# Optimization experiments

Hardware: AMD Instinct MI355X
Metric: run time of the kernel (lower is better)

Reference implementation:

```python
import jax, jax.numpy as jnp
import numpy as np

B, V, NB, K = 4, 5023, 10, 9
# (Cin, Cout) per NLayer: encoder Linear(3->16) then 3 encoder NLayers, 3 decoder NLayers, Linear(3->3)
CH = [(16, 16), (16, 16), (16, 32), (32, 16), (16, 16), (16, 3)]


def _glorot(key, shape):
    fan_in, fan_out = shape[0], shape[-1]
    s = np.float32(np.sqrt(2.0 / (fan_in + fan_out)))
    return (jax.random.normal(key, shape, dtype=jnp.float32) * s)


def setup_inputs():
    key = jax.random.key(0)
    ks = jax.random.split(key, 4 + 4 * len(CH))
    inp = {}
    inp["x"] = jax.random.normal(ks[0], (B, V, 3), dtype=jnp.float32)
    inp["adj"] = jax.random.randint(ks[1], (V, NB), 0, V + 1, dtype=jnp.int32)
    inp["Win"] = _glorot(ks[2], (3, CH[0][0]))
    inp["Wout"] = _glorot(ks[3], (CH[-1][1], 3))
    for i, (cin, cout) in enumerate(CH):
        k0, k1, k2, k3 = ks[4 + 4 * i], ks[5 + 4 * i], ks[6 + 4 * i], ks[7 + 4 * i]
        inp[f"W{i}"] = _glorot(k0, (cin, K, cout))
        inp[f"b{i}"] = jax.random.normal(k1, (cout,), dtype=jnp.float32) * 0.01
        inp[f"u{i}"] = _glorot(k2, (cin, K))
        inp[f"c{i}"] = jax.random.normal(k3, (K,), dtype=jnp.float32) * 0.01
    return inp


def _pad_gather(t, adj):
    # t: [B, V, ...]; pad a zero row at vertex index 0, gather neighbor features.
    z = jnp.zeros(t.shape[:1] + (1,) + t.shape[2:], t.dtype)
    return jnp.take(jnp.concatenate([z, t], axis=1), adj, axis=1)  # [B, V, NB, ...]


def _nlayer(h, adj, recip, W, b, u, c):
    # h: [B, V, Cin], W: [Cin, K, Cout], u: [Cin, K]
    wx = jnp.einsum('bvc,cko->bvko', h, W)          # [B, V, K, Cout]
    nb_w = _pad_gather(wx, adj)                      # [B, V, NB, K, Cout]
    ux = jnp.einsum('bvc,ck->bvk', h, u)             # [B, V, K]  (u and v maps share self.u)
    nb_u = _pad_gather(ux, adj)                      # [B, V, NB, K]
    q = jax.nn.softmax(ux[:, :, None, :] + nb_u + c, axis=-1)  # softmax over kernel dim
    out = jnp.einsum('bvnk,bvnko->bvo', q, nb_w)     # sum over neighbors & kernels
    return out * recip[None, :, None] + b


def reference(x, adj, Win, Wout, W0, b0, u0, c0, W1, b1, u1, c1, W2, b2, u2, c2,
              W3, b3, u3, c3, W4, b4, u4, c4, W5, b5, u5, c5):
    cnt = jnp.sum(adj != 0, axis=-1).astype(jnp.float32)        # [V]
    recip = jnp.where(cnt > 0, 1.0 / jnp.maximum(cnt, 1.0), 0.0)
    h = jax.nn.relu(x @ Win)
    layers = [(W0, b0, u0, c0), (W1, b1, u1, c1), (W2, b2, u2, c2),
              (W3, b3, u3, c3), (W4, b4, u4, c4), (W5, b5, u5, c5)]
    for (W, b, u, c) in layers:
        h = jax.nn.relu(_nlayer(h, adj, recip, W, b, u, c))
    return h @ Wout
```

## Files before the change

kernel.cpp:

```cpp
#include <hip/hip_runtime.h>

#define NBK 10
#define KK  9

constexpr int Bv  = 4;
constexpr int Vv  = 5023;
constexpr int TOT = Bv * Vv;


__device__ __forceinline__ float merge16(float* a, int t)
{
#pragma unroll
    for (int j = 0; j < 8; j++) {
        float send = (t & 8) ? a[j] : a[j + 8];
        float keep = (t & 8) ? a[j + 8] : a[j];
        a[j] = keep + __shfl_xor(send, 8, 16);
    }
#pragma unroll
    for (int j = 0; j < 4; j++) {
        float send = (t & 4) ? a[j] : a[j + 4];
        float keep = (t & 4) ? a[j + 4] : a[j];
        a[j] = keep + __shfl_xor(send, 4, 16);
    }
#pragma unroll
    for (int j = 0; j < 2; j++) {
        float send = (t & 2) ? a[j] : a[j + 2];
        float keep = (t & 2) ? a[j + 2] : a[j];
        a[j] = keep + __shfl_xor(send, 2, 16);
    }
    {
        float send = (t & 1) ? a[0] : a[1];
        float keep = (t & 1) ? a[1] : a[0];
        a[0] = keep + __shfl_xor(send, 1, 16);
    }
    return a[0];
}

__global__ __launch_bounds__(256, 4) void enc_l0_kernel(
    const float* __restrict__ x,
    const int*   __restrict__ adj,
    const float* __restrict__ Win,
    const float* __restrict__ u0,
    const float* __restrict__ W,
    const float* __restrict__ bvec,
    const float* __restrict__ cvec,
    const float* __restrict__ unx,
    float* __restrict__ hux_out)
{
    constexpr int COUTP = 20;
    __shared__ __align__(16) float s_w[KK * 16 * COUTP];

    const int tid = threadIdx.x;

    {
        constexpr int NF4 = 16 * KK * 16 / 4;
        constexpr int KC4 = KK * 16 / 4;
        const float4* W4 = reinterpret_cast<const float4*>(W);
        for (int i = tid; i < NF4; i += 256) {
            const int c   = i / KC4;
            const int rem = i - c * KC4;
            const int k   = rem >> 2;
            const int o4  = rem & 3;
            *reinterpret_cast<float4*>(&s_w[(k * 16 + c) * COUTP + o4 * 4]) = W4[i];
        }
    }
    __syncthreads();

    const int g = tid >> 4;
    const int t = tid & 15;
    const int vv = blockIdx.x * 16 + g;
    if (vv >= TOT) return;
    const int b = vv / Vv;
    const int v = vv - b * Vv;
    const float* xB = x + (size_t)b * Vv * 3;

    int nb[NBK];
    const int2* arow = reinterpret_cast<const int2*>(&adj[v * NBK]);
#pragma unroll
    for (int j = 0; j < 5; j++) { int2 p = arow[j]; nb[2 * j] = p.x; nb[2 * j + 1] = p.y; }
    int cnt = 0;
#pragma unroll
    for (int n = 0; n < NBK; n++) cnt += (nb[n] != 0) ? 1 : 0;
    const float rec = cnt ? (1.0f / (float)cnt) : 0.0f;

    const float w0 = Win[t], w1 = Win[16 + t], w2 = Win[32 + t];
    float hn0[NBK];
#pragma unroll
    for (int n = 0; n < NBK; n++) {
        const int a = nb[n];
        float x0 = 0.f, x1 = 0.f, x2 = 0.f;
        if (a) {
            const float* xr = &xB[(size_t)(a - 1) * 3];
            x0 = xr[0]; x1 = xr[1]; x2 = xr[2];
        }
        hn0[n] = fmaxf(x0 * w0 + x1 * w1 + x2 * w2, 0.0f);
    }

    float q[KK] = {};
    if (t < NBK) {
        const float* xo = &xB[(size_t)v * 3];
        const float xo0 = xo[0], xo1 = xo[1], xo2 = xo[2];
        const int a = nb[t];
        float xn0 = 0.f, xn1 = 0.f, xn2 = 0.f;
        if (a) {
            const float* xr = &xB[(size_t)(a - 1) * 3];
            xn0 = xr[0]; xn1 = xr[1]; xn2 = xr[2];
        }
        float hs[16];
#pragma unroll
        for (int c = 0; c < 16; c++) {
            const float ho = fmaxf(xo0 * Win[c] + xo1 * Win[16 + c] + xo2 * Win[32 + c], 0.0f);
            const float hn = fmaxf(xn0 * Win[c] + xn1 * Win[16 + c] + xn2 * Win[32 + c], 0.0f);
            hs[c] = ho + hn;
        }
        float lg[KK];
#pragma unroll
        for (int k = 0; k < KK; k++) {
            float s = cvec[k];
#pragma unroll
            for (int c = 0; c < 16; c++) s = fmaf(hs[c], u0[c * KK + k], s);
            lg[k] = s;
        }
        float m = lg[0];
#pragma unroll
        for (int k = 1; k < KK; k++) m = fmaxf(m, lg[k]);
        float sum = 0.0f;
#pragma unroll
        for (int k = 0; k < KK; k++) { q[k] = __expf(lg[k] - m); sum += q[k]; }
        const float r = 1.0f / sum;
#pragma unroll
        for (int k = 0; k < KK; k++) q[k] *= r;
    }

    float g0[KK];
#pragma unroll
    for (int k = 0; k < KK; k++) g0[k] = 0.0f;
#pragma unroll
    for (int n = 0; n < NBK; n++) {
#pragma unroll
        for (int k = 0; k < KK; k++) {
            const float qnk = __shfl(q[k], n, 16);
            g0[k] = fmaf(qnk, hn0[n], g0[k]);
        }
    }

    float acc[16] = {};
#pragma unroll
    for (int k = 0; k < KK; k++) {
        const float g0k = g0[k];
        const float* wr = &s_w[(k * 16 + t) * COUTP];
#pragma unroll
        for (int o4 = 0; o4 < 4; o4++) {
            const float4 w = *reinterpret_cast<const float4*>(&wr[4 * o4]);
            acc[4 * o4 + 0] = fmaf(g0k, w.x, acc[4 * o4 + 0]);
            acc[4 * o4 + 1] = fmaf(g0k, w.y, acc[4 * o4 + 1]);
            acc[4 * o4 + 2] = fmaf(g0k, w.z, acc[4 * o4 + 2]);
            acc[4 * o4 + 3] = fmaf(g0k, w.w, acc[4 * o4 + 3]);
        }
    }

    const float o0 = merge16(acc, t);
    const float h0v = fmaxf(fmaf(o0, rec, bvec[t]), 0.0f);
    float* row = &hux_out[(size_t)vv * 32];
    row[t] = h0v;

    float uxv = 0.0f;
#pragma unroll
    for (int o = 0; o < 16; o++) {
        const float hb = __shfl(h0v, o, 16);
        if (t < KK) uxv = fmaf(hb, unx[o * KK + t], uxv);
    }
    if (t < KK) row[16 + t] = uxv;
}

template<int CIN, int COUT, bool LAST, int RSI, int RSO>
__global__ __launch_bounds__(256) void nlayer_kernel(
    const float* __restrict__ hux_in,
    const int*   __restrict__ adj,
    const float* __restrict__ W,
    const float* __restrict__ bvec,
    const float* __restrict__ cvec,
    const float* __restrict__ unx,
    float* __restrict__ hux_out,
    float* __restrict__ dout)
{
    constexpr int COUTP = (COUT == 32) ? 36 : ((COUT == 16) ? 20 : 4);

    __shared__ __align__(16) float s_w[KK * CIN * COUTP];
    __shared__ __align__(16) float s_q[16][NBK][12];

    const int tid = threadIdx.x;
    const int g = tid >> 4;
    const int t = tid & 15;
    const int vv = blockIdx.x * 16 + g;
    const bool act = vv < TOT;
    int b = 0, v = 0;
    if (act) { b = vv / Vv; v = vv - b * Vv; }
    const float* inB = hux_in + (size_t)b * Vv * RSI;

    int nb[NBK];
    if (act) {
        const int2* arow = reinterpret_cast<const int2*>(&adj[v * NBK]);
#pragma unroll
        for (int j = 0; j < 5; j++) { int2 p = arow[j]; nb[2 * j] = p.x; nb[2 * j + 1] = p.y; }
    } else {
#pragma unroll
        for (int n = 0; n < NBK; n++) nb[n] = 0;
    }
    int cnt = 0;
#pragma unroll
    for (int n = 0; n < NBK; n++) cnt += (nb[n] != 0) ? 1 : 0;
    const float rec = cnt ? (1.0f / (float)cnt) : 0.0f;

    float hn0[NBK], hn1[NBK];
#pragma unroll
    for (int n = 0; n < NBK; n++) {
        const int a = nb[n];
        const float* r = &inB[(size_t)(a - 1) * RSI];
        hn0[n] = a ? r[t] : 0.0f;
        if constexpr (CIN == 32) hn1[n] = a ? r[t + 16] : 0.0f;
        else                     hn1[n] = 0.0f;
    }

    float4 s0 = make_float4(0.f, 0.f, 0.f, 0.f), s1 = s0, n0 = s0, n1 = s0;
    float  s8 = 0.f, n8 = 0.f;
    if (t < NBK) {
        const float* su = &inB[(size_t)v * RSI + CIN];
        s0 = *reinterpret_cast<const float4*>(su);
        s1 = *reinterpret_cast<const float4*>(su + 4);
        s8 = su[8];
        const int a = nb[t];
        if (a) {
            const float* nu = &inB[(size_t)(a - 1) * RSI + CIN];
            n0 = *reinterpret_cast<const float4*>(nu);
            n1 = *reinterpret_cast<const float4*>(nu + 4);
            n8 = nu[8];
        }
    }

    if constexpr (!LAST) {
        constexpr int NF4 = CIN * KK * COUT / 4;
        constexpr int KC4 = KK * COUT / 4;
        constexpr int C4  = COUT / 4;
        const float4* W4 = reinterpret_cast<const float4*>(W);
        for (int i = tid; i < NF4; i += 256) {
            const int c   = i / KC4;
            const int rem = i - c * KC4;
            const int k   = rem / C4;
            const int o4  = rem - k * C4;
            *reinterpret_cast<float4*>(&s_w[(k * CIN + c) * COUTP + o4 * 4]) = W4[i];
        }
    } else {
        for (int i = tid; i < CIN * KK * 3; i += 256) {
            const int c   = i / (KK * 3);
            const int rem = i - c * (KK * 3);
            const int k   = rem / 3;
            const int o   = rem - k * 3;
            s_w[(k * CIN + c) * COUTP + o] = W[i];
        }
    }
    __syncthreads();
    if (!act) return;

    if (t < NBK) {
        float lg[KK] = { s0.x + n0.x + cvec[0], s0.y + n0.y + cvec[1],
                         s0.z + n0.z + cvec[2], s0.w + n0.w + cvec[3],
                         s1.x + n1.x + cvec[4], s1.y + n1.y + cvec[5],
                         s1.z + n1.z + cvec[6], s1.w + n1.w + cvec[7],
                         s8 + n8 + cvec[8] };
        float m = lg[0];
#pragma unroll
        for (int k = 1; k < KK; k++) m = fmaxf(m, lg[k]);
        float e[KK], sum = 0.0f;
#pragma unroll
        for (int k = 0; k < KK; k++) { e[k] = __expf(lg[k] - m); sum += e[k]; }
        const float r = 1.0f / sum;
        *reinterpret_cast<float4*>(&s_q[g][t][0]) =
            make_float4(e[0] * r, e[1] * r, e[2] * r, e[3] * r);
        *reinterpret_cast<float4*>(&s_q[g][t][4]) =
            make_float4(e[4] * r, e[5] * r, e[6] * r, e[7] * r);
        s_q[g][t][8] = e[8] * r;
    }

    float g0[KK], g1[KK];
#pragma unroll
    for (int k = 0; k < KK; k++) { g0[k] = 0.0f; g1[k] = 0.0f; }
#pragma unroll
    for (int n = 0; n < NBK; n++) {
        const float4 qa = *reinterpret_cast<const float4*>(&s_q[g][n][0]);
        const float4 qb = *reinterpret_cast<const float4*>(&s_q[g][n][4]);
        const float  q8 = s_q[g][n][8];
        const float h0 = hn0[n];
        g0[0] = fmaf(qa.x, h0, g0[0]); g0[1] = fmaf(qa.y, h0, g0[1]);
        g0[2] = fmaf(qa.z, h0, g0[2]); g0[3] = fmaf(qa.w, h0, g0[3]);
        g0[4] = fmaf(qb.x, h0, g0[4]); g0[5] = fmaf(qb.y, h0, g0[5]);
        g0[6] = fmaf(qb.z, h0, g0[6]); g0[7] = fmaf(qb.w, h0, g0[7]);
        g0[8] = fmaf(q8,   h0, g0[8]);
        if constexpr (CIN == 32) {
            const float h1 = hn1[n];
            g1[0] = fmaf(qa.x, h1, g1[0]); g1[1] = fmaf(qa.y, h1, g1[1]);
            g1[2] = fmaf(qa.z, h1, g1[2]); g1[3] = fmaf(qa.w, h1, g1[3]);
            g1[4] = fmaf(qb.x, h1, g1[4]); g1[5] = fmaf(qb.y, h1, g1[5]);
            g1[6] = fmaf(qb.z, h1, g1[6]); g1[7] = fmaf(qb.w, h1, g1[7]);
            g1[8] = fmaf(q8,   h1, g1[8]);
        }
    }

    if constexpr (!LAST) {
        float acc[COUT] = {};
#pragma unroll
        for (int k = 0; k < KK; k++) {
            const float g0k = g0[k];
            const float* wr = &s_w[(k * CIN + t) * COUTP];
#pragma unroll
            for (int o4 = 0; o4 < COUT / 4; o4++) {
                const float4 w = *reinterpret_cast<const float4*>(&wr[4 * o4]);
                acc[4 * o4 + 0] = fmaf(g0k, w.x, acc[4 * o4 + 0]);
                acc[4 * o4 + 1] = fmaf(g0k, w.y, acc[4 * o4 + 1]);
                acc[4 * o4 + 2] = fmaf(g0k, w.z, acc[4 * o4 + 2]);
                acc[4 * o4 + 3] = fmaf(g0k, w.w, acc[4 * o4 + 3]);
            }
            if constexpr (CIN == 32) {
                const float g1k = g1[k];
                const float* wr2 = &s_w[(k * CIN + t + 16) * COUTP];
#pragma unroll
                for (int o4 = 0; o4 < COUT / 4; o4++) {
                    const float4 w = *reinterpret_cast<const float4*>(&wr2[4 * o4]);
                    acc[4 * o4 + 0] = fmaf(g1k, w.x, acc[4 * o4 + 0]);
                    acc[4 * o4 + 1] = fmaf(g1k, w.y, acc[4 * o4 + 1]);
                    acc[4 * o4 + 2] = fmaf(g1k, w.z, acc[4 * o4 + 2]);
                    acc[4 * o4 + 3] = fmaf(g1k, w.w, acc[4 * o4 + 3]);
                }
            }
        }

        const float o0 = merge16(acc, t);
        const float h0v = fmaxf(fmaf(o0, rec, bvec[t]), 0.0f);
        float* row = &hux_out[(size_t)vv * RSO];
        row[t] = h0v;
        float h1v = 0.0f;
        if constexpr (COUT == 32) {
            const float o1 = merge16(acc + 16, t);
            h1v = fmaxf(fmaf(o1, rec, bvec[t + 16]), 0.0f);
            row[16 + t] = h1v;
        }

        float uxv = 0.0f;
#pragma unroll
        for (int o = 0; o < 16; o++) {
            const float hb = __shfl(h0v, o, 16);
            if (t < KK) uxv = fmaf(hb, unx[o * KK + t], uxv);
        }
        if constexpr (COUT == 32) {
#pragma unroll
            for (int o = 0; o < 16; o++) {
                const float hb = __shfl(h1v, o, 16);
                if (t < KK) uxv = fmaf(hb, unx[(o + 16) * KK + t], uxv);
            }
        }
        if (t < KK) row[COUT + t] = uxv;
    } else {
        float acc[3] = {};
#pragma unroll
        for (int k = 0; k < KK; k++) {
            const float4 w = *reinterpret_cast<const float4*>(&s_w[(k * CIN + t) * COUTP]);
            acc[0] = fmaf(g0[k], w.x, acc[0]);
            acc[1] = fmaf(g0[k], w.y, acc[1]);
            acc[2] = fmaf(g0[k], w.z, acc[2]);
        }
#pragma unroll
        for (int o = 0; o < 3; o++) {
            acc[o] += __shfl_xor(acc[o], 1, 16);
            acc[o] += __shfl_xor(acc[o], 2, 16);
            acc[o] += __shfl_xor(acc[o], 4, 16);
            acc[o] += __shfl_xor(acc[o], 8, 16);
        }
        float hnew[3];
#pragma unroll
        for (int o = 0; o < 3; o++)
            hnew[o] = fmaxf(fmaf(acc[o], rec, bvec[o]), 0.0f);
        if (t < 3) {
            float s = 0.0f;
#pragma unroll
            for (int j = 0; j < 3; j++)
                s = fmaf(hnew[j], unx[j * 3 + t], s);
            dout[(size_t)vv * 3 + t] = s;
        }
    }
}

extern "C" void kernel_launch(void* const* d_in, const int* in_sizes, int n_in,
                              void* d_out, int out_size, void* d_ws, size_t ws_size,
                              hipStream_t stream)
{
    const float* x    = (const float*)d_in[0];
    const int*   adj  = (const int*)  d_in[1];
    const float* Win  = (const float*)d_in[2];
    const float* Wout = (const float*)d_in[3];
    const float *W[6], *bb[6], *uu[6], *cc[6];
    for (int i = 0; i < 6; i++) {
        W[i]  = (const float*)d_in[4 + 4 * i];
        bb[i] = (const float*)d_in[5 + 4 * i];
        uu[i] = (const float*)d_in[6 + 4 * i];
        cc[i] = (const float*)d_in[7 + 4 * i];
    }
    float* out = (float*)d_out;

    float* p  = (float*)d_ws;
    float* B1 = p; p += (size_t)TOT * 32;
    float* B2 = p; p += (size_t)TOT * 32;
    float* B3 = p; p += (size_t)TOT * 48;
    float* B4 = p; p += (size_t)TOT * 32;
    float* B5 = p; p += (size_t)TOT * 32;

    const int nb = (TOT + 15) / 16;

    enc_l0_kernel<<<nb, 256, 0, stream>>>(x, adj, Win, uu[0], W[0], bb[0], cc[0],
                                          uu[1], B1);
    nlayer_kernel<16, 16, false, 32, 32><<<nb, 256, 0, stream>>>(B1, adj, W[1], bb[1], cc[1], uu[2], B2, nullptr);
    nlayer_kernel<16, 32, false, 32, 48><<<nb, 256, 0, stream>>>(B2, adj, W[2], bb[2], cc[2], uu[3], B3, nullptr);
    nlayer_kernel<32, 16, false, 48, 32><<<nb, 256, 0, stream>>>(B3, adj, W[3], bb[3], cc[3], uu[4], B4, nullptr);
    nlayer_kernel<16, 16, false, 32, 32><<<nb, 256, 0, stream>>>(B4, adj, W[4], bb[4], cc[4], uu[5], B5, nullptr);
    nlayer_kernel<16, 3, true, 32, 32><<<nb, 256, 0, stream>>>(B5, adj, W[5], bb[5], cc[5], Wout, nullptr, out);
}
```

Before: 76.73 us.

## Process two vertices per 16-lane group in nlayer kernels to reuse weights

Each 16-thread group in the nlayer kernels now handles two vertices instead of one, so each block covers 32 vertices. The weight tile is staged into shared memory once per 32 vertices instead of 16, and every shared-memory weight read feeds two accumulator sets. Launch bounds gain a min-blocks hint of 3 and the grid is halved. The cost is doubled register arrays (gathered neighbours, accumulators), which may cause spills or lower occupancy, and fewer blocks, which may leave CUs underfilled.

Result: slower. 226.9 us (+195.7%).

```diff
diff --git a/kernel.cpp b/kernel.cpp
--- a/kernel.cpp
+++ b/kernel.cpp
@@ -37,14 +37,10 @@
 }
 
 __global__ __launch_bounds__(256, 4) void enc_l0_kernel(
-    const float* __restrict__ x,
-    const int*   __restrict__ adj,
-    const float* __restrict__ Win,
-    const float* __restrict__ u0,
-    const float* __restrict__ W,
-    const float* __restrict__ bvec,
-    const float* __restrict__ cvec,
-    const float* __restrict__ unx,
+    const float* __restrict__ x, const int* __restrict__ adj,
+    const float* __restrict__ Win, const float* __restrict__ u0,
+    const float* __restrict__ W, const float* __restrict__ bvec,
+    const float* __restrict__ cvec, const float* __restrict__ unx,
     float* __restrict__ hux_out)
 {
     constexpr int COUTP = 20;
@@ -174,7 +170,7 @@
 }
 
 template<int CIN, int COUT, bool LAST, int RSI, int RSO>
-__global__ __launch_bounds__(256) void nlayer_kernel(
+__global__ __launch_bounds__(256, 3) void nlayer2_kernel(
     const float* __restrict__ hux_in,
     const int*   __restrict__ adj,
     const float* __restrict__ W,
@@ -187,54 +183,53 @@
     constexpr int COUTP = (COUT == 32) ? 36 : ((COUT == 16) ? 20 : 4);
 
     __shared__ __align__(16) float s_w[KK * CIN * COUTP];
-    __shared__ __align__(16) float s_q[16][NBK][12];
+    __shared__ __align__(16) float s_q[32][NBK][12];
 
     const int tid = threadIdx.x;
     const int g = tid >> 4;
     const int t = tid & 15;
-    const int vv = blockIdx.x * 16 + g;
-    const bool act = vv < TOT;
-    int b = 0, v = 0;
-    if (act) { b = vv / Vv; v = vv - b * Vv; }
-    const float* inB = hux_in + (size_t)b * Vv * RSI;
-
-    int nb[NBK];
-    if (act) {
-        const int2* arow = reinterpret_cast<const int2*>(&adj[v * NBK]);
-#pragma unroll
-        for (int j = 0; j < 5; j++) { int2 p = arow[j]; nb[2 * j] = p.x; nb[2 * j + 1] = p.y; }
-    } else {
-#pragma unroll
-        for (int n = 0; n < NBK; n++) nb[n] = 0;
-    }
-    int cnt = 0;
-#pragma unroll
-    for (int n = 0; n < NBK; n++) cnt += (nb[n] != 0) ? 1 : 0;
-    const float rec = cnt ? (1.0f / (float)cnt) : 0.0f;
-
-    float hn0[NBK], hn1[NBK];
-#pragma unroll
-    for (int n = 0; n < NBK; n++) {
-        const int a = nb[n];
-        const float* r = &inB[(size_t)(a - 1) * RSI];
-        hn0[n] = a ? r[t] : 0.0f;
-        if constexpr (CIN == 32) hn1[n] = a ? r[t + 16] : 0.0f;
-        else                     hn1[n] = 0.0f;
-    }
-
-    float4 s0 = make_float4(0.f, 0.f, 0.f, 0.f), s1 = s0, n0 = s0, n1 = s0;
-    float  s8 = 0.f, n8 = 0.f;
-    if (t < NBK) {
-        const float* su = &inB[(size_t)v * RSI + CIN];
-        s0 = *reinterpret_cast<const float4*>(su);
-        s1 = *reinterpret_cast<const float4*>(su + 4);
-        s8 = su[8];
-        const int a = nb[t];
-        if (a) {
-            const float* nu = &inB[(size_t)(a - 1) * RSI + CIN];
-            n0 = *reinterpret_cast<const float4*>(nu);
-            n1 = *reinterpret_cast<const float4*>(nu + 4);
-            n8 = nu[8];
+
+    int  vvA[2], bA[2], vA[2];
+    bool actA[2];
+    vvA[0] = blockIdx.x * 32 + g;
+    vvA[1] = vvA[0] + 16;
+#pragma unroll
+    for (int it = 0; it < 2; ++it) {
+        actA[it] = vvA[it] < TOT;
+        const int vvc = actA[it] ? vvA[it] : 0;
+        bA[it] = vvc / Vv;
+        vA[it] = vvc - bA[it] * Vv;
+    }
+
+    int   nb[2][NBK];
+    float hn0[2][NBK], hn1[2][NBK];
+    float recA[2];
+#pragma unroll
+    for (int it = 0; it < 2; ++it) {
+        if (actA[it]) {
+            const int2* arow = reinterpret_cast<const int2*>(&adj[vA[it] * NBK]);
+#pragma unroll
+            for (int j = 0; j < 5; j++) {
+                int2 p = arow[j];
+                nb[it][2 * j] = p.x; nb[it][2 * j + 1] = p.y;
+            }
+        } else {
+#pragma unroll
+            for (int n = 0; n < NBK; n++) nb[it][n] = 0;
+        }
+        int cnt = 0;
+#pragma unroll
+        for (int n = 0; n < NBK; n++) cnt += (nb[it][n] != 0) ? 1 : 0;
+        recA[it] = cnt ? (1.0f / (float)cnt) : 0.0f;
+
+        const float* inB = hux_in + (size_t)bA[it] * Vv * RSI;
+#pragma unroll
+        for (int n = 0; n < NBK; n++) {
+            const int a = nb[it][n];
+            const float* r = &inB[(size_t)(a - 1) * RSI];
+            hn0[it][n] = a ? r[t] : 0.0f;
+            if constexpr (CIN == 32) hn1[it][n] = a ? r[t + 16] : 0.0f;
+            else                     hn1[it][n] = 0.0f;
         }
     }
 
@@ -260,131 +255,191 @@
         }
     }
     __syncthreads();
-    if (!act) return;
 
     if (t < NBK) {
-        float lg[KK] = { s0.x + n0.x + cvec[0], s0.y + n0.y + cvec[1],
-                         s0.z + n0.z + cvec[2], s0.w + n0.w + cvec[3],
-                         s1.x + n1.x + cvec[4], s1.y + n1.y + cvec[5],
-                         s1.z + n1.z + cvec[6], s1.w + n1.w + cvec[7],
-                         s8 + n8 + cvec[8] };
-        float m = lg[0];
-#pragma unroll
-        for (int k = 1; k < KK; k++) m = fmaxf(m, lg[k]);
-        float e[KK], sum = 0.0f;
-#pragma unroll
-        for (int k = 0; k < KK; k++) { e[k] = __expf(lg[k] - m); sum += e[k]; }
-        const float r = 1.0f / sum;
-        *reinterpret_cast<float4*>(&s_q[g][t][0]) =
-            make_float4(e[0] * r, e[1] * r, e[2] * r, e[3] * r);
-        *reinterpret_cast<float4*>(&s_q[g][t][4]) =
-            make_float4(e[4] * r, e[5] * r, e[6] * r, e[7] * r);
-        s_q[g][t][8] = e[8] * r;
-    }
-
-    float g0[KK], g1[KK];
-#pragma unroll
-    for (int k = 0; k < KK; k++) { g0[k] = 0.0f; g1[k] = 0.0f; }
-#pragma unroll
-    for (int n = 0; n < NBK; n++) {
-        const float4 qa = *reinterpret_cast<const float4*>(&s_q[g][n][0]);
-        const float4 qb = *reinterpret_cast<const float4*>(&s_q[g][n][4]);
-        const float  q8 = s_q[g][n][8];
-        const float h0 = hn0[n];
-        g0[0] = fmaf(qa.x, h0, g0[0]); g0[1] = fmaf(qa.y, h0, g0[1]);
-        g0[2] = fmaf(qa.z, h0, g0[2]); g0[3] = fmaf(qa.w, h0, g0[3]);
-        g0[4] = fmaf(qb.x, h0, g0[4]); g0[5] = fmaf(qb.y, h0, g0[5]);
-        g0[6] = fmaf(qb.z, h0, g0[6]); g0[7] = fmaf(qb.w, h0, g0[7]);
-        g0[8] = fmaf(q8,   h0, g0[8]);
-        if constexpr (CIN == 32) {
-            const float h1 = hn1[n];
-            g1[0] = fmaf(qa.x, h1, g1[0]); g1[1] = fmaf(qa.y, h1, g1[1]);
-            g1[2] = fmaf(qa.z, h1, g1[2]); g1[3] = fmaf(qa.w, h1, g1[3]);
-            g1[4] = fmaf(qb.x, h1, g1[4]); g1[5] = fmaf(qb.y, h1, g1[5]);
-            g1[6] = fmaf(qb.z, h1, g1[6]); g1[7] = fmaf(qb.w, h1, g1[7]);
-            g1[8] = fmaf(q8,   h1, g1[8]);
+#pragma unroll
+        for (int it = 0; it < 2; ++it) {
+            const float* inB = hux_in + (size_t)bA[it] * Vv * RSI;
+            const float* su = &inB[(size_t)vA[it] * RSI + CIN];
+            const float4 s0 = *reinterpret_cast<const float4*>(su);
+            const float4 s1 = *reinterpret_cast<const float4*>(su + 4);
+            const float  s8 = su[8];
+            const int a = nb[it][t];
+            float4 n0 = make_float4(0.f, 0.f, 0.f, 0.f), n1 = n0;
+            float  n8 = 0.0f;
+            if (a) {
+                const float* nu = &inB[(size_t)(a - 1) * RSI + CIN];
+                n0 = *reinterpret_cast<const float4*>(nu);
+                n1 = *reinterpret_cast<const float4*>(nu + 4);
+                n8 = nu[8];
+            }
+            float lg[KK] = { s0.x + n0.x + cvec[0], s0.y + n0.y + cvec[1],
+                             s0.z + n0.z + cvec[2], s0.w + n0.w + cvec[3],
+                             s1.x + n1.x + cvec[4], s1.y + n1.y + cvec[5],
+                             s1.z + n1.z + cvec[6], s1.w + n1.w + cvec[7],
+                             s8 + n8 + cvec[8] };
+            float m = lg[0];
+#pragma unroll
+            for (int k = 1; k < KK; k++) m = fmaxf(m, lg[k]);
+            float e[KK], sum = 0.0f;
+#pragma unroll
+            for (int k = 0; k < KK; k++) { e[k] = __expf(lg[k] - m); sum += e[k]; }
+            const float r = 1.0f / sum;
+            float* qd = &s_q[g + 16 * it][t][0];
+            *reinterpret_cast<float4*>(qd) =
+                make_float4(e[0] * r, e[1] * r, e[2] * r, e[3] * r);
+            *reinterpret_cast<float4*>(qd + 4) =
+                make_float4(e[4] * r, e[5] * r, e[6] * r, e[7] * r);
+            qd[8] = e[8] * r;
+        }
+    }
+
+    float g0[2][KK], g1[2][KK];
+#pragma unroll
+    for (int it = 0; it < 2; ++it)
+#pragma unroll
+        for (int k = 0; k < KK; k++) { g0[it][k] = 0.0f; g1[it][k] = 0.0f; }
+#pragma unroll
+    for (int it = 0; it < 2; ++it) {
+#pragma unroll
+        for (int n = 0; n < NBK; n++) {
+            const float4 qa = *reinterpret_cast<const float4*>(&s_q[g + 16 * it][n][0]);
+            const float4 qb = *reinterpret_cast<const float4*>(&s_q[g + 16 * it][n][4]);
+            const float  q8 = s_q[g + 16 * it][n][8];
+            const float h0 = hn0[it][n];
+            g0[it][0] = fmaf(qa.x, h0, g0[it][0]); g0[it][1] = fmaf(qa.y, h0, g0[it][1]);
+            g0[it][2] = fmaf(qa.z, h0, g0[it][2]); g0[it][3] = fmaf(qa.w, h0, g0[it][3]);
+            g0[it][4] = fmaf(qb.x, h0, g0[it][4]); g0[it][5] = fmaf(qb.y, h0, g0[it][5]);
+            g0[it][6] = fmaf(qb.z, h0, g0[it][6]); g0[it][7] = fmaf(qb.w, h0, g0[it][7]);
+            g0[it][8] = fmaf(q8,   h0, g0[it][8]);
+            if constexpr (CIN == 32) {
+                const float h1 = hn1[it][n];
+                g1[it][0] = fmaf(qa.x, h1, g1[it][0]); g1[it][1] = fmaf(qa.y, h1, g1[it][1]);
+                g1[it][2] = fmaf(qa.z, h1, g1[it][2]); g1[it][3] = fmaf(qa.w, h1, g1[it][3]);
+                g1[it][4] = fmaf(qb.x, h1, g1[it][4]); g1[it][5] = fmaf(qb.y, h1, g1[it][5]);
+                g1[it][6] = fmaf(qb.z, h1, g1[it][6]); g1[it][7] = fmaf(qb.w, h1, g1[it][7]);
+                g1[it][8] = fmaf(q8,   h1, g1[it][8]);
+            }
         }
     }
 
     if constexpr (!LAST) {
-        float acc[COUT] = {};
+        float acc0[COUT] = {}, acc1[COUT] = {};
 #pragma unroll
         for (int k = 0; k < KK; k++) {
-            const float g0k = g0[k];
+            const float a0 = g0[0][k], a1 = g0[1][k];
             const float* wr = &s_w[(k * CIN + t) * COUTP];
 #pragma unroll
             for (int o4 = 0; o4 < COUT / 4; o4++) {
                 const float4 w = *reinterpret_cast<const float4*>(&wr[4 * o4]);
-                acc[4 * o4 + 0] = fmaf(g0k, w.x, acc[4 * o4 + 0]);
-                acc[4 * o4 + 1] = fmaf(g0k, w.y, acc[4 * o4 + 1]);
-                acc[4 * o4 + 2] = fmaf(g0k, w.z, acc[4 * o4 + 2]);
-                acc[4 * o4 + 3] = fmaf(g0k, w.w, acc[4 * o4 + 3]);
+                acc0[4 * o4 + 0] = fmaf(a0, w.x, acc0[4 * o4 + 0]);
+                acc0[4 * o4 + 1] = fmaf(a0, w.y, acc0[4 * o4 + 1]);
+                acc0[4 * o4 + 2] = fmaf(a0, w.z, acc0[4 * o4 + 2]);
+                acc0[4 * o4 + 3] = fmaf(a0, w.w, acc0[4 * o4 + 3]);
+                acc1[4 * o4 + 0] = fmaf(a1, w.x, acc1[4 * o4 + 0]);
+                acc1[4 * o4 + 1] = fmaf(a1, w.y, acc1[4 * o4 + 1]);
+                acc1[4 * o4 + 2] = fmaf(a1, w.z, acc1[4 * o4 + 2]);
+                acc1[4 * o4 + 3] = fmaf(a1, w.w, acc1[4 * o4 + 3]);
             }
             if constexpr (CIN == 32) {
-                const float g1k = g1[k];
+                const float b0 = g1[0][k], b1 = g1[1][k];
                 const float* wr2 = &s_w[(k * CIN + t + 16) * COUTP];
 #pragma unroll
                 for (int o4 = 0; o4 < COUT / 4; o4++) {
                     const float4 w = *reinterpret_cast<const float4*>(&wr2[4 * o4]);
-                    acc[4 * o4 + 0] = fmaf(g1k, w.x, acc[4 * o4 + 0]);
-                    acc[4 * o4 + 1] = fmaf(g1k, w.y, acc[4 * o4 + 1]);
-                    acc[4 * o4 + 2] = fmaf(g1k, w.z, acc[4 * o4 + 2]);
-                    acc[4 * o4 + 3] = fmaf(g1k, w.w, acc[4 * o4 + 3]);
+                    acc0[4 * o4 + 0] = fmaf(b0, w.x, acc0[4 * o4 + 0]);
+                    acc0[4 * o4 + 1] = fmaf(b0, w.y, acc0[4 * o4 + 1]);
+                    acc0[4 * o4 + 2] = fmaf(b0, w.z, acc0[4 * o4 + 2]);
+                    acc0[4 * o4 + 3] = fmaf(b0, w.w, acc0[4 * o4 + 3]);
+                    acc1[4 * o4 + 0] = fmaf(b1, w.x, acc1[4 * o4 + 0]);
+                    acc1[4 * o4 + 1] = fmaf(b1, w.y, acc1[4 * o4 + 1]);
+                    acc1[4 * o4 + 2] = fmaf(b1, w.z, acc1[4 * o4 + 2]);
+                    acc1[4 * o4 + 3] = fmaf(b1, w.w, acc1[4 * o4 + 3]);
                 }
             }
         }
 
-        const float o0 = merge16(acc, t);
-        const float h0v = fmaxf(fmaf(o0, rec, bvec[t]), 0.0f);
-        float* row = &hux_out[(size_t)vv * RSO];
-        row[t] = h0v;
-        float h1v = 0.0f;
+        const float o00 = merge16(acc0, t);
+        const float h0v0 = fmaxf(fmaf(o00, recA[0], bvec[t]), 0.0f);
+        float h1v0 = 0.0f;
+        if (actA[0]) hux_out[(size_t)vvA[0] * RSO + t] = h0v0;
         if constexpr (COUT == 32) {
-            const float o1 = merge16(acc + 16, t);
-            h1v = fmaxf(fmaf(o1, rec, bvec[t + 16]), 0.0f);
-            row[16 + t] = h1v;
-        }
-
-        float uxv = 0.0f;
+            const float o10 = merge16(acc0 + 16, t);
+            h1v0 = fmaxf(fmaf(o10, recA[0], bvec[t + 16]), 0.0f);
+            if (actA[0]) hux_out[(size_t)vvA[0] * RSO + 16 + t] = h1v0;
+        }
+        const float o01 = merge16(acc1, t);
+        const float h0v1 = fmaxf(fmaf(o01, recA[1], bvec[t]), 0.0f);
+        float h1v1 = 0.0f;
+        if (actA[1]) hux_out[(size_t)vvA[1] * RSO + t] = h0v1;
+        if constexpr (COUT == 32) {
+            const float o11 = merge16(acc1 + 16, t);
+            h1v1 = fmaxf(fmaf(o11, recA[1], bvec[t + 16]), 0.0f);
+            if (actA[1]) hux_out[(size_t)vvA[1] * RSO + 16 + t] = h1v1;
+        }
+
+        float uxv0 = 0.0f, uxv1 = 0.0f;
 #pragma unroll
         for (int o = 0; o < 16; o++) {
-            const float hb = __shfl(h0v, o, 16);
-            if (t < KK) uxv = fmaf(hb, unx[o * KK + t], uxv);
+            const float un = (t < KK) ? unx[o * KK + t] : 0.0f;
+            const float hb0 = __shfl(h0v0, o, 16);
+            const float hb1 = __shfl(h0v1, o, 16);
+            uxv0 = fmaf(hb0, un, uxv0);
+            uxv1 = fmaf(hb1, un, uxv1);
         }
         if constexpr (COUT == 32) {
 #pragma unroll
             for (int o = 0; o < 16; o++) {
-                const float hb = __shfl(h1v, o, 16);
-                if (t < KK) uxv = fmaf(hb, unx[(o + 16) * KK + t], uxv);
-            }
-        }
-        if (t < KK) row[COUT + t] = uxv;
+                const float un = (t < KK) ? unx[(o + 16) * KK + t] : 0.0f;
+                const float hb0 = __shfl(h1v0, o, 16);
+                const float hb1 = __shfl(h1v1, o, 16);
+                uxv0 = fmaf(hb0, un, uxv0);
+                uxv1 = fmaf(hb1, un, uxv1);
+            }
+        }
+        if (t < KK) {
+            if (actA[0]) hux_out[(size_t)vvA[0] * RSO + COUT + t] = uxv0;
+            if (actA[1]) hux_out[(size_t)vvA[1] * RSO + COUT + t] = uxv1;
+        }
     } else {
-        float acc[3] = {};
+        float acc0[3] = {}, acc1[3] = {};
 #pragma unroll
         for (int k = 0; k < KK; k++) {
             const float4 w = *reinterpret_cast<const float4*>(&s_w[(k * CIN + t) * COUTP]);
-            acc[0] = fmaf(g0[k], w.x, acc[0]);
-            acc[1] = fmaf(g0[k], w.y, acc[1]);
-            acc[2] = fmaf(g0[k], w.z, acc[2]);
+            acc0[0] = fmaf(g0[0][k], w.x, acc0[0]);
+            acc0[1] = fmaf(g0[0][k], w.y, acc0[1]);
+            acc0[2] = fmaf(g0[0][k], w.z, acc0[2]);
+            acc1[0] = fmaf(g0[1][k], w.x, acc1[0]);
+            acc1[1] = fmaf(g0[1][k], w.y, acc1[1]);
+            acc1[2] = fmaf(g0[1][k], w.z, acc1[2]);
         }
 #pragma unroll
         for (int o = 0; o < 3; o++) {
-            acc[o] += __shfl_xor(acc[o], 1, 16);
-            acc[o] += __shfl_xor(acc[o], 2, 16);
-            acc[o] += __shfl_xor(acc[o], 4, 16);
-            acc[o] += __shfl_xor(acc[o], 8, 16);
-        }
-        float hnew[3];
-#pragma unroll
-        for (int o = 0; o < 3; o++)
-            hnew[o] = fmaxf(fmaf(acc[o], rec, bvec[o]), 0.0f);
+            acc0[o] += __shfl_xor(acc0[o], 1, 16);
+            acc0[o] += __shfl_xor(acc0[o], 2, 16);
+            acc0[o] += __shfl_xor(acc0[o], 4, 16);
+            acc0[o] += __shfl_xor(acc0[o], 8, 16);
+            acc1[o] += __shfl_xor(acc1[o], 1, 16);
+            acc1[o] += __shfl_xor(acc1[o], 2, 16);
+            acc1[o] += __shfl_xor(acc1[o], 4, 16);
+            acc1[o] += __shfl_xor(acc1[o], 8, 16);
+        }
+        float hnew0[3], hnew1[3];
+#pragma unroll
+        for (int o = 0; o < 3; o++) {
+            hnew0[o] = fmaxf(fmaf(acc0[o], recA[0], bvec[o]), 0.0f);
+            hnew1[o] = fmaxf(fmaf(acc1[o], recA[1], bvec[o]), 0.0f);
+        }
         if (t < 3) {
-            float s = 0.0f;
-#pragma unroll
-            for (int j = 0; j < 3; j++)
-                s = fmaf(hnew[j], unx[j * 3 + t], s);
-            dout[(size_t)vv * 3 + t] = s;
+            float s0 = 0.0f, s1 = 0.0f;
+#pragma unroll
+            for (int j = 0; j < 3; j++) {
+                const float un = unx[j * 3 + t];
+                s0 = fmaf(hnew0[j], un, s0);
+                s1 = fmaf(hnew1[j], un, s1);
+            }
+            if (actA[0]) dout[(size_t)vvA[0] * 3 + t] = s0;
+            if (actA[1]) dout[(size_t)vvA[1] * 3 + t] = s1;
         }
     }
 }
@@ -413,13 +468,14 @@
     float* B4 = p; p += (size_t)TOT * 32;
     float* B5 = p; p += (size_t)TOT * 32;
 
-    const int nb = (TOT + 15) / 16;
-
-    enc_l0_kernel<<<nb, 256, 0, stream>>>(x, adj, Win, uu[0], W[0], bb[0], cc[0],
-                                          uu[1], B1);
-    nlayer_kernel<16, 16, false, 32, 32><<<nb, 256, 0, stream>>>(B1, adj, W[1], bb[1], cc[1], uu[2], B2, nullptr);
-    nlayer_kernel<16, 32, false, 32, 48><<<nb, 256, 0, stream>>>(B2, adj, W[2], bb[2], cc[2], uu[3], B3, nullptr);
-    nlayer_kernel<32, 16, false, 48, 32><<<nb, 256, 0, stream>>>(B3, adj, W[3], bb[3], cc[3], uu[4], B4, nullptr);
-    nlayer_kernel<16, 16, false, 32, 32><<<nb, 256, 0, stream>>>(B4, adj, W[4], bb[4], cc[4], uu[5], B5, nullptr);
-    nlayer_kernel<16, 3, true, 32, 32><<<nb, 256, 0, stream>>>(B5, adj, W[5], bb[5], cc[5], Wout, nullptr, out);
+    const int nb1 = (TOT + 15) / 16;
+    const int nb2 = (TOT + 31) / 32;
+
+    enc_l0_kernel<<<nb1, 256, 0, stream>>>(x, adj, Win, uu[0], W[0], bb[0], cc[0],
+                                           uu[1], B1);
+    nlayer2_kernel<16, 16, false, 32, 32><<<nb2, 256, 0, stream>>>(B1, adj, W[1], bb[1], cc[1], uu[2], B2, nullptr);
+    nlayer2_kernel<16, 32, false, 32, 48><<<nb2, 256, 0, stream>>>(B2, adj, W[2], bb[2], cc[2], uu[3], B3, nullptr);
+    nlayer2_kernel<32, 16, false, 48, 32><<<nb2, 256, 0, stream>>>(B3, adj, W[3], bb[3], cc[3], uu[4], B4, nullptr);
+    nlayer2_kernel<16, 16, false, 32, 32><<<nb2, 256, 0, stream>>>(B4, adj, W[4], bb[4], cc[4], uu[5], B5, nullptr);
+    nlayer2_kernel<16, 3, true, 32, 32><<<nb2, 256, 0, stream>>>(B5, adj, W[5], bb[5], cc[5], Wout, nullptr, out);
 }
```
